# Performance work log

Measured on AMD Instinct MI355X. Metric: run time of the kernel, lower is better.

## Reference

```python
import jax, jax.numpy as jnp
import numpy as np

# E2M1 (FP4) representable magnitudes and rounding midpoints
LEVELS = jnp.array([0.0, 0.5, 1.0, 1.5, 2.0, 3.0, 4.0, 6.0], dtype=jnp.float32)
BOUNDS = jnp.array([0.25, 0.75, 1.25, 1.75, 2.5, 3.5, 5.0], dtype=jnp.float32)
E2M1_MAX = 6.0
EPS = 1e-12


def e2m1_block_quant_dequant(x, block_size):
    """Block-wise E2M1 fake-quantization along the last dim.

    Per block of `block_size` elements: scale = absmax / 6.0, then
    round-to-nearest onto the E2M1 grid {0,.5,1,1.5,2,3,4,6} (signed)
    and dequantize. Returns (dequantized x, per-block scales).
    """
    shape = x.shape
    nb = shape[-1] // block_size
    xb = x.reshape(*shape[:-1], nb, block_size)
    amax = jnp.max(jnp.abs(xb), axis=-1, keepdims=True)          # [..., nb, 1]
    scale = jnp.maximum(amax / E2M1_MAX, EPS)
    v = xb / scale
    mag = jnp.abs(v)
    # nearest E2M1 level: count how many rounding boundaries |v| exceeds
    idx = jnp.sum((mag[..., None] > BOUNDS).astype(jnp.int32), axis=-1)
    q = jnp.sign(v) * LEVELS[idx] * scale                        # dequantized
    return q.reshape(shape), scale[..., 0]


def setup_inputs() -> dict:
    key = jax.random.key(0)
    k1, k2, k3 = jax.random.split(key, 3)
    x = jax.random.normal(k1, (8, 1500, 1280), dtype=jnp.float32)
    weight = jax.random.normal(k2, (5120, 1280), dtype=jnp.float32) * 0.02
    bias = jax.random.normal(k3, (5120,), dtype=jnp.float32) * 0.01
    return {"x": x, "weight": weight, "bias": bias}


def reference(x, weight, bias):
    # activation quant (block_size_act = 32, along feature dim)
    x_q, _ = e2m1_block_quant_dequant(x, 32)
    # weight quant (block_size_w = 32, along in_features dim)
    w_q, scale_w = e2m1_block_quant_dequant(weight, 32)
    # F.linear: x @ W^T + b
    out = jnp.einsum('bsi,oi->bso', x_q, w_q) + bias
    return (out, scale_w)
```

## Files before the change

kernel.cpp:

```cpp
#include <hip/hip_runtime.h>
#include <hip/hip_fp16.h>


typedef _Float16 f16;
typedef _Float16 f16x8 __attribute__((ext_vector_type(8)));
typedef float f32x4 __attribute__((ext_vector_type(4)));

#define M_ROWS 12000
#define M_PAD  12032
#define N_COLS 5120
#define K_DIM  1280
#define KB     40
#define NTN    20

#define BAR()   asm volatile("s_barrier" ::: "memory")
#define VMCNT(N) asm volatile("s_waitcnt vmcnt(%0)" :: "i"(N) : "memory")
#define GLDS(gp, lp) __builtin_amdgcn_global_load_lds( \
    (const __attribute__((address_space(1))) unsigned*)(gp), \
    (__attribute__((address_space(3))) unsigned*)(lp), 16, 0, 0)

__device__ __forceinline__ float e2m1_level(float a) {
    float lv;
    if (a > 2.5f)       lv = (a > 3.5f) ? ((a > 5.0f) ? 6.0f : 4.0f) : 3.0f;
    else if (a > 1.25f) lv = (a > 1.75f) ? 2.0f : 1.5f;
    else                lv = (a > 0.75f) ? 1.0f : ((a > 0.25f) ? 0.5f : 0.0f);
    return lv;
}

__global__ __launch_bounds__(256) void quant_x_kernel(const float* __restrict__ x,
                                                      f16* __restrict__ xq) {
    int t = blockIdx.x * blockDim.x + threadIdx.x;
    int row = t / 160;
    int c8  = t % 160;
    f16x8 o;
    if (row < M_ROWS) {
        const float* p = x + (size_t)row * K_DIM + c8 * 8;
        float v[8];
        *(float4*)&v[0] = *(const float4*)p;
        *(float4*)&v[4] = *(const float4*)(p + 4);
        float am = 0.0f;
        #pragma unroll
        for (int i = 0; i < 8; ++i) am = fmaxf(am, fabsf(v[i]));
        am = fmaxf(am, __shfl_xor(am, 1));
        am = fmaxf(am, __shfl_xor(am, 2));
        float scale = fmaxf(am / 6.0f, 1e-12f);
        #pragma unroll
        for (int i = 0; i < 8; ++i) {
            float tq = v[i] / scale;
            float q  = copysignf(e2m1_level(fabsf(tq)), tq) * scale;
            o[i] = (f16)q;
        }
    } else {
        #pragma unroll
        for (int i = 0; i < 8; ++i) o[i] = (f16)0.0f;
    }
    *(f16x8*)(xq + (size_t)row * K_DIM + c8 * 8) = o;
}

__global__ __launch_bounds__(256) void quant_w_kernel(const float* __restrict__ w,
                                                      f16* __restrict__ wq,
                                                      float* __restrict__ scale_out) {
    int t = blockIdx.x * blockDim.x + threadIdx.x;
    int row = t / 160;
    int c8  = t % 160;
    const float* p = w + (size_t)row * K_DIM + c8 * 8;
    float v[8];
    *(float4*)&v[0] = *(const float4*)p;
    *(float4*)&v[4] = *(const float4*)(p + 4);
    float am = 0.0f;
    #pragma unroll
    for (int i = 0; i < 8; ++i) am = fmaxf(am, fabsf(v[i]));
    am = fmaxf(am, __shfl_xor(am, 1));
    am = fmaxf(am, __shfl_xor(am, 2));
    float scale = fmaxf(am / 6.0f, 1e-12f);
    if ((t & 3) == 0) scale_out[row * KB + (c8 >> 2)] = scale;
    f16x8 o;
    #pragma unroll
    for (int i = 0; i < 8; ++i) {
        float tq = v[i] / scale;
        float q  = copysignf(e2m1_level(fabsf(tq)), tq) * scale;
        o[i] = (f16)q;
    }
    *(f16x8*)(wq + (size_t)row * K_DIM + c8 * 8) = o;
}


__device__ __forceinline__ void stage_half(const f16* __restrict__ g, f16* l, int tid) {
    #pragma unroll
    for (int s = 0; s < 2; ++s) {
        int j = s * 512 + tid;
        int r = j >> 3;
        int c = (j & 7) ^ (r & 7);
        GLDS(g + (size_t)r * K_DIM + c * 8, l + (size_t)j * 8);
    }
}

#define READ_A(dst, buf, rbase)                                                \
    _Pragma("unroll")                                                          \
    for (int fm = 0; fm < 4; ++fm) {                                           \
        dst[fm][0] = *(const f16x8*)&(buf)[((rbase) + fm * 16) * 64 + swz[0]]; \
        dst[fm][1] = *(const f16x8*)&(buf)[((rbase) + fm * 16) * 64 + swz[1]]; \
    }
#define READ_B(dst, buf, rbase)                                                \
    _Pragma("unroll")                                                          \
    for (int fn = 0; fn < 2; ++fn) {                                           \
        dst[fn][0] = *(const f16x8*)&(buf)[((rbase) + fn * 16) * 64 + swz[0]]; \
        dst[fn][1] = *(const f16x8*)&(buf)[((rbase) + fn * 16) * 64 + swz[1]]; \
    }
#define MFMA_Q(ma, mb, mo, no)                                                 \
    __builtin_amdgcn_s_setprio(1);                                             \
    _Pragma("unroll")                                                          \
    for (int fm = 0; fm < 4; ++fm)                                             \
        _Pragma("unroll")                                                      \
        for (int fn = 0; fn < 2; ++fn) {                                       \
            acc[fm + mo][fn + no] = __builtin_amdgcn_mfma_f32_16x16x32_f16(    \
                ma[fm][0], mb[fn][0], acc[fm + mo][fn + no], 0, 0, 0);         \
            acc[fm + mo][fn + no] = __builtin_amdgcn_mfma_f32_16x16x32_f16(    \
                ma[fm][1], mb[fn][1], acc[fm + mo][fn + no], 0, 0, 0);         \
        }                                                                      \
    __builtin_amdgcn_s_setprio(0);

template<int PAR, bool STAGE, bool VM, bool READNEXT>
__device__ __forceinline__ void ktile(f16* Xa, f16* Xb,
                                      const f16* Ya, const f16* Yb,
                                      const f16* gA2, const f16* gB2,
                                      f16x8 (&aLO)[4][2], f16x8 (&bLO)[2][2][2],
                                      f32x4 (&acc)[8][4],
                                      int tid, int arow0, int brow0, const int (&swz)[2]) {
    f16x8 bHI[2][2], aHI[4][2];

    READ_B(bHI, Xb, brow0 + 32);
    MFMA_Q(aLO, bLO[PAR], 0, 0);
    BAR();

    READ_A(aHI, Xa, arow0 + 64);
    MFMA_Q(aLO, bHI, 0, 2);
    if (VM) VMCNT(0);
    BAR();

    if (STAGE) { stage_half(gB2, Xb, tid); stage_half(gB2 + 128 * K_DIM, Xb + 8192, tid); }
    if (READNEXT) { READ_A(aLO, Ya, arow0); }
    MFMA_Q(aHI, bHI, 4, 2);
    BAR();

    if (STAGE) { stage_half(gA2, Xa, tid); stage_half(gA2 + 128 * K_DIM, Xa + 8192, tid); }
    if (READNEXT) { READ_B(bLO[1 - PAR], Yb, brow0); }
    MFMA_Q(aHI, bLO[PAR], 4, 0);
    BAR();
}

__global__ __launch_bounds__(512, 2) void gemm_kernel(const f16* __restrict__ A,
                                                      const f16* __restrict__ B,
                                                      const float* __restrict__ bias,
                                                      float* __restrict__ C) {
    extern __shared__ f16 sm[];
    int mt = blockIdx.x / NTN;
    int nt = blockIdx.x % NTN;

    int tid  = threadIdx.x;
    int lane = tid & 63;
    int wid  = tid >> 6;
    int wr   = wid >> 2;
    int wc   = wid & 3;
    int l15  = lane & 15;

    int swz[2] = { (((lane >> 4)    ) ^ (lane & 7)) * 8,
                   (((lane >> 4) + 4) ^ (lane & 7)) * 8 };
    int arow0 = wr * 128 + l15;
    int brow0 = wc * 64 + l15;

    const f16* gAb = A + (size_t)(mt * 256) * K_DIM;
    const f16* gBb = B + (size_t)(nt * 256) * K_DIM;

    f16* A0 = sm;
    f16* B0 = sm + 16384;
    f16* A1 = sm + 32768;
    f16* B1 = sm + 49152;

    f32x4 acc[8][4] = {};
    f16x8 aLO[4][2];
    f16x8 bLO[2][2][2];

    stage_half(gAb,               A0,        tid);
    stage_half(gAb + 128 * K_DIM, A0 + 8192, tid);
    stage_half(gBb,               B0,        tid);
    stage_half(gBb + 128 * K_DIM, B0 + 8192, tid);
    stage_half(gAb + 64,               A1,        tid);
    stage_half(gAb + 64 + 128 * K_DIM, A1 + 8192, tid);
    stage_half(gBb + 64,               B1,        tid);
    stage_half(gBb + 64 + 128 * K_DIM, B1 + 8192, tid);
    VMCNT(8);
    BAR();
    READ_A(aLO, A0, arow0);
    READ_B(bLO[0], B0, brow0);

    for (int tt = 0; tt < 9; ++tt) {
        int t = 2 * tt;
        ktile<0, true, true, true>(A0, B0, A1, B1,
                                   gAb + (t + 2) * 64, gBb + (t + 2) * 64,
                                   aLO, bLO, acc, tid, arow0, brow0, swz);
        ktile<1, true, true, true>(A1, B1, A0, B0,
                                   gAb + (t + 3) * 64, gBb + (t + 3) * 64,
                                   aLO, bLO, acc, tid, arow0, brow0, swz);
    }
    ktile<0, false, true, true>(A0, B0, A1, B1, gAb, gBb,
                                aLO, bLO, acc, tid, arow0, brow0, swz);
    ktile<1, false, false, false>(A1, B1, A0, B0, gAb, gBb,
                                  aLO, bLO, acc, tid, arow0, brow0, swz);

    int crow0 = mt * 256 + wr * 128;
    int ccol  = nt * 256 + wc * 64 + l15;
    float bz[4];
    #pragma unroll
    for (int fn = 0; fn < 4; ++fn) bz[fn] = bias[ccol + fn * 16];

    #pragma unroll
    for (int fm = 0; fm < 8; ++fm) {
        #pragma unroll
        for (int j = 0; j < 4; ++j) {
            int row = crow0 + fm * 16 + (lane >> 4) * 4 + j;
            if (row < M_ROWS) {
                float* cp = C + (size_t)row * N_COLS + ccol;
                #pragma unroll
                for (int fn = 0; fn < 4; ++fn)
                    cp[fn * 16] = acc[fm][fn][j] + bz[fn];
            }
        }
    }
}

extern "C" void kernel_launch(void* const* d_in, const int* in_sizes, int n_in,
                              void* d_out, int out_size, void* d_ws, size_t ws_size,
                              hipStream_t stream) {
    const float* x      = (const float*)d_in[0];
    const float* weight = (const float*)d_in[1];
    const float* bias   = (const float*)d_in[2];
    float* out     = (float*)d_out;
    float* scale_w = (float*)d_out + (size_t)M_ROWS * N_COLS;

    f16* xq = (f16*)d_ws;
    f16* wq = (f16*)((char*)d_ws + (size_t)M_PAD * K_DIM * sizeof(f16));

    (void)hipFuncSetAttribute((const void*)gemm_kernel,
                              hipFuncAttributeMaxDynamicSharedMemorySize, 131072);

    {
        int threads = M_PAD * (K_DIM / 8);
        quant_x_kernel<<<threads / 256, 256, 0, stream>>>(x, xq);
    }
    {
        int threads = N_COLS * (K_DIM / 8);
        quant_w_kernel<<<threads / 256, 256, 0, stream>>>(weight, wq, scale_w);
    }
    {
        int grid = (M_PAD / 256) * (N_COLS / 256);
        gemm_kernel<<<grid, 512, 131072, stream>>>(xq, wq, bias, out);
    }
}
```

Baseline: 233.5 us.

## Restructure GEMM k-tile schedule to two barriers with earlier staging and partial vmcnt

Rewrites the per-k-tile schedule of the FP16 MFMA GEMM. Each k-tile now uses two barriers instead of four. B fragments are read fully at the start of the tile instead of being carried across tiles, and the A high half is read in two split pieces interleaved with the MFMAs. The next B tile is issued earlier, and the wait becomes vmcnt(4) instead of vmcnt(0), so A loads can stay in flight longer. The goal is less barrier stall and better overlap of global-to-LDS copies with compute, at the cost of a riskier ordering between LDS reads and the overwriting global_load_lds.

```diff
diff --git a/kernel.cpp b/kernel.cpp
--- a/kernel.cpp
+++ b/kernel.cpp
@@ -120,33 +120,44 @@
         }                                                                      \
     __builtin_amdgcn_s_setprio(0);
 
-template<int PAR, bool STAGE, bool VM, bool READNEXT>
-__device__ __forceinline__ void ktile(f16* Xa, f16* Xb,
-                                      const f16* Ya, const f16* Yb,
+template<int PAR, bool STAGE, int VM, bool READNEXT>
+__device__ __forceinline__ void ktile(f16* Xa, f16* Xb, const f16* Ya,
                                       const f16* gA2, const f16* gB2,
-                                      f16x8 (&aLO)[4][2], f16x8 (&bLO)[2][2][2],
+                                      f16x8 (&aLO)[4][2],
                                       f32x4 (&acc)[8][4],
                                       int tid, int arow0, int brow0, const int (&swz)[2]) {
-    f16x8 bHI[2][2], aHI[4][2];
-
+    f16x8 bLO[2][2], bHI[2][2], aHI[4][2];
+
+    READ_B(bLO, Xb, brow0);
     READ_B(bHI, Xb, brow0 + 32);
-    MFMA_Q(aLO, bLO[PAR], 0, 0);
+    MFMA_Q(aLO, bLO, 0, 0);
+
+    #pragma unroll
+    for (int fm = 0; fm < 4; ++fm)
+        aHI[fm][0] = *(const f16x8*)&Xa[(arow0 + 64 + fm * 16) * 64 + swz[0]];
+    MFMA_Q(aLO, bHI, 0, 2);
     BAR();
 
-    READ_A(aHI, Xa, arow0 + 64);
-    MFMA_Q(aLO, bHI, 0, 2);
-    if (VM) VMCNT(0);
+    if (STAGE) { stage_half(gB2, Xb, tid); stage_half(gB2 + 128 * K_DIM, Xb + 8192, tid); }
+    #pragma unroll
+    for (int fm = 0; fm < 4; ++fm)
+        aHI[fm][1] = *(const f16x8*)&Xa[(arow0 + 64 + fm * 16) * 64 + swz[1]];
+    __builtin_amdgcn_s_setprio(1);
+    #pragma unroll
+    for (int ks = 0; ks < 2; ++ks)
+        #pragma unroll
+        for (int fm = 0; fm < 4; ++fm)
+            #pragma unroll
+            for (int fn = 0; fn < 2; ++fn)
+                acc[fm + 4][fn + 2] = __builtin_amdgcn_mfma_f32_16x16x32_f16(
+                    aHI[fm][ks], bHI[fn][ks], acc[fm + 4][fn + 2], 0, 0, 0);
+    __builtin_amdgcn_s_setprio(0);
+    if (VM >= 0) { if (VM == 4) VMCNT(4); else VMCNT(0); }
     BAR();
 
-    if (STAGE) { stage_half(gB2, Xb, tid); stage_half(gB2 + 128 * K_DIM, Xb + 8192, tid); }
+    if (STAGE) { stage_half(gA2, Xa, tid); stage_half(gA2 + 128 * K_DIM, Xa + 8192, tid); }
     if (READNEXT) { READ_A(aLO, Ya, arow0); }
-    MFMA_Q(aHI, bHI, 4, 2);
-    BAR();
-
-    if (STAGE) { stage_half(gA2, Xa, tid); stage_half(gA2 + 128 * K_DIM, Xa + 8192, tid); }
-    if (READNEXT) { READ_B(bLO[1 - PAR], Yb, brow0); }
-    MFMA_Q(aHI, bLO[PAR], 4, 0);
-    BAR();
+    MFMA_Q(aHI, bLO, 4, 0);
 }
 
 __global__ __launch_bounds__(512, 2) void gemm_kernel(const f16* __restrict__ A,
@@ -179,7 +190,6 @@
 
     f32x4 acc[8][4] = {};
     f16x8 aLO[4][2];
-    f16x8 bLO[2][2][2];
 
     stage_half(gAb,               A0,        tid);
     stage_half(gAb + 128 * K_DIM, A0 + 8192, tid);
@@ -192,21 +202,20 @@
     VMCNT(8);
     BAR();
     READ_A(aLO, A0, arow0);
-    READ_B(bLO[0], B0, brow0);
 
     for (int tt = 0; tt < 9; ++tt) {
         int t = 2 * tt;
-        ktile<0, true, true, true>(A0, B0, A1, B1,
-                                   gAb + (t + 2) * 64, gBb + (t + 2) * 64,
-                                   aLO, bLO, acc, tid, arow0, brow0, swz);
-        ktile<1, true, true, true>(A1, B1, A0, B0,
-                                   gAb + (t + 3) * 64, gBb + (t + 3) * 64,
-                                   aLO, bLO, acc, tid, arow0, brow0, swz);
-    }
-    ktile<0, false, true, true>(A0, B0, A1, B1, gAb, gBb,
-                                aLO, bLO, acc, tid, arow0, brow0, swz);
-    ktile<1, false, false, false>(A1, B1, A0, B0, gAb, gBb,
-                                  aLO, bLO, acc, tid, arow0, brow0, swz);
+        ktile<0, true, 4, true>(A0, B0, A1,
+                                gAb + (t + 2) * 64, gBb + (t + 2) * 64,
+                                aLO, acc, tid, arow0, brow0, swz);
+        ktile<1, true, 4, true>(A1, B1, A0,
+                                gAb + (t + 3) * 64, gBb + (t + 3) * 64,
+                                aLO, acc, tid, arow0, brow0, swz);
+    }
+    ktile<0, false, 0, true>(A0, B0, A1, gAb, gBb,
+                             aLO, acc, tid, arow0, brow0, swz);
+    ktile<1, false, -1, false>(A1, B1, A0, gAb, gBb,
+                               aLO, acc, tid, arow0, brow0, swz);
 
     int crow0 = mt * 256 + wr * 128;
     int ccol  = nt * 256 + wc * 64 + l15;
```

New measurement: 195.0 us. 16.5% less time.
